# Performance work log

Measured on AMD Instinct MI355X. Metric: run time of the kernel, lower is better.

The kernel has to match this reference:

```python
import jax, jax.numpy as jnp
import numpy as np

DIM = 1024
HEADS = 16
HEAD_DIM = DIM // HEADS
MAX_SEQ = 4096
BATCH = 16
POSITION = MAX_SEQ - 1


def setup_inputs() -> dict:
    key = jax.random.key(0)
    ks = jax.random.split(key, 8)
    s = 0.02  # weight init scale, typical for transformer linears
    return {
        "token": jax.random.normal(ks[0], (BATCH, 1, DIM), dtype=jnp.float32),
        "k_cache": jax.random.normal(ks[1], (BATCH, MAX_SEQ, HEADS, HEAD_DIM), dtype=jnp.float32),
        "v_cache": jax.random.normal(ks[2], (BATCH, MAX_SEQ, HEADS, HEAD_DIM), dtype=jnp.float32),
        "Wq": jax.random.normal(ks[3], (DIM, DIM), dtype=jnp.float32) * s,
        "Wk": jax.random.normal(ks[4], (DIM, DIM), dtype=jnp.float32) * s,
        "Wv": jax.random.normal(ks[5], (DIM, DIM), dtype=jnp.float32) * s,
        "Wo": jax.random.normal(ks[6], (DIM, DIM), dtype=jnp.float32) * s,
        "position": POSITION,
    }


def reference(token, k_cache, v_cache, Wq, Wk, Wv, Wo, position):
    # Decode step: single-query attention against KV cache (FlexDecodingModule.decode).
    B = token.shape[0]
    # QKV projections (torch Linear: x @ W.T), bias=False
    q = (token @ Wq.T).reshape(B, 1, HEADS, HEAD_DIM)
    k = (token @ Wk.T).reshape(B, 1, HEADS, HEAD_DIM)
    v = (token @ Wv.T).reshape(B, 1, HEADS, HEAD_DIM)
    # Inline KV-cache append at `position` (static python int)
    kc = k_cache.at[:, position].set(k[:, 0])
    vc = v_cache.at[:, position].set(v[:, 0])
    past_k = kc[:, : position + 1]  # [B, L, H, D]
    past_v = vc[:, : position + 1]
    # Causal score_mod with offset=position, q_idx=0 => all kv_idx<=position visible (no mask)
    scale = 1.0 / np.sqrt(HEAD_DIM).astype(np.float32)
    scores = jnp.einsum("bqhd,bkhd->bhqk", q, past_k) * scale  # [B, H, 1, L]
    attn = jax.nn.softmax(scores, axis=-1)
    out = jnp.einsum("bhqk,bkhd->bqhd", attn, past_v)  # [B, 1, H, D]
    out = out.reshape(B, 1, DIM)
    return out @ Wo.T
```

## Files before the change

kernel.cpp:

```cpp
#include <hip/hip_runtime.h>
#include <hip/hip_bf16.h>
#include <math.h>

#define DIM 1024
#define HEADS 16
#define HEAD_DIM 64
#define MAXSEQ 4096
#define BATCH 16
#define CHUNK 64
#define NCHUNK (MAXSEQ / CHUNK)

__global__ __launch_bounds__(256) void qkv_proj(
    const float* __restrict__ token,
    const float* __restrict__ Wq, const float* __restrict__ Wk,
    const float* __restrict__ Wv,
    float* __restrict__ out ) {
  __shared__ float tok[BATCH * DIM];
  for (int idx = threadIdx.x; idx < BATCH * DIM; idx += 256)
    tok[idx] = token[idx];
  __syncthreads();

  const float* W = (blockIdx.y == 0) ? Wq : ((blockIdx.y == 1) ? Wk : Wv);
  float* o = out + (size_t)blockIdx.y * BATCH * DIM;

  const int wave = threadIdx.x >> 6;
  const int lane = threadIdx.x & 63;
  const int i0 = blockIdx.x * 16 + wave * 4;

  float acc[4][16];
#pragma unroll
  for (int ii = 0; ii < 4; ++ii)
#pragma unroll
    for (int b = 0; b < 16; ++b) acc[ii][b] = 0.f;

  for (int t = 0; t < 16; ++t) {
    const int j = t * 64 + lane;
    float tk[16];
#pragma unroll
    for (int b = 0; b < 16; ++b) tk[b] = tok[b * DIM + j];
#pragma unroll
    for (int ii = 0; ii < 4; ++ii) {
      const float w = W[(size_t)(i0 + ii) * DIM + j];
#pragma unroll
      for (int b = 0; b < 16; ++b) acc[ii][b] = fmaf(w, tk[b], acc[ii][b]);
    }
  }

#pragma unroll
  for (int ii = 0; ii < 4; ++ii)
#pragma unroll
    for (int b = 0; b < 16; ++b) {
      float v = acc[ii][b];
#pragma unroll
      for (int m = 32; m >= 1; m >>= 1) v += __shfl_xor(v, m);
      if (lane == 0) o[(size_t)b * DIM + i0 + ii] = v;
    }
}

__global__ __launch_bounds__(256) void attn_partial(
    const float* __restrict__ kc, const float* __restrict__ vc,
    const float* __restrict__ qkv, const int* __restrict__ pos_p,
    float* __restrict__ part) {
  const int c = blockIdx.x, b = blockIdx.y;
  const int t = threadIdx.x;
  const int h = t >> 4, lq = t & 15;
  const int pos = pos_p[0];
  const int nk = pos + 1;
  const int s0 = c * CHUNK;

  const float* qp   = qkv + (size_t)b * DIM;
  const float* knew = qkv + (size_t)BATCH * DIM + (size_t)b * DIM;
  const float* vnew = qkv + 2 * (size_t)BATCH * DIM + (size_t)b * DIM;
  const float* kbase = kc + (size_t)b * MAXSEQ * DIM;
  const float* vbase = vc + (size_t)b * MAXSEQ * DIM;

  const float scale = 0.125f;
  float4 q4 = *(const float4*)(qp + 4 * t);
  q4.x *= scale; q4.y *= scale; q4.z *= scale; q4.w *= scale;

  __shared__ float sc[CHUNK][17];

#pragma unroll 4
  for (int i = 0; i < CHUNK; ++i) {
    const int s = s0 + i;
    const bool valid = (s < nk);
    float d = 0.f;
    if (valid) {
      const float* krow = (s == pos) ? knew : (kbase + (size_t)s * DIM);
      const float4 k4 = *(const float4*)(krow + 4 * t);
      d = q4.x * k4.x + q4.y * k4.y + q4.z * k4.z + q4.w * k4.w;
      d += __shfl_xor(d, 1);
      d += __shfl_xor(d, 2);
      d += __shfl_xor(d, 4);
      d += __shfl_xor(d, 8);
    }
    if (lq == 0) sc[i][h] = valid ? d : -INFINITY;
  }
  __syncthreads();

  float m = -INFINITY;
#pragma unroll
  for (int r = 0; r < CHUNK / 16; ++r)
    m = fmaxf(m, sc[lq * (CHUNK / 16) + r][h]);
  m = fmaxf(m, __shfl_xor(m, 1));
  m = fmaxf(m, __shfl_xor(m, 2));
  m = fmaxf(m, __shfl_xor(m, 4));
  m = fmaxf(m, __shfl_xor(m, 8));

  float l = 0.f;
#pragma unroll
  for (int r = 0; r < CHUNK / 16; ++r) {
    const int i = lq * (CHUNK / 16) + r;
    const float sv = sc[i][h];
    const float p = (sv == -INFINITY) ? 0.f : __expf(sv - m);
    l += p;
    sc[i][h] = p;
  }
  l += __shfl_xor(l, 1);
  l += __shfl_xor(l, 2);
  l += __shfl_xor(l, 4);
  l += __shfl_xor(l, 8);
  __syncthreads();

  float4 a4 = make_float4(0.f, 0.f, 0.f, 0.f);
#pragma unroll 4
  for (int i = 0; i < CHUNK; ++i) {
    const int s = s0 + i;
    if (s < nk) {
      const float* vrow = (s == pos) ? vnew : (vbase + (size_t)s * DIM);
      const float4 v4 = *(const float4*)(vrow + 4 * t);
      const float p = sc[i][h];
      a4.x = fmaf(p, v4.x, a4.x);
      a4.y = fmaf(p, v4.y, a4.y);
      a4.z = fmaf(p, v4.z, a4.z);
      a4.w = fmaf(p, v4.w, a4.w);
    }
  }

  const size_t base = (((size_t)(b * HEADS + h)) * NCHUNK + c) * 66;
  part[base + 2 + lq * 4 + 0] = a4.x;
  part[base + 2 + lq * 4 + 1] = a4.y;
  part[base + 2 + lq * 4 + 2] = a4.z;
  part[base + 2 + lq * 4 + 3] = a4.w;
  if (lq == 0) { part[base] = m; part[base + 1] = l; }
}

__global__ __launch_bounds__(64) void attn_combine(
    const float* __restrict__ part, float* __restrict__ attn) {
  const int bh = blockIdx.x;
  const int b = bh >> 4, h = bh & 15;
  const int d = threadIdx.x;
  const float* p0 = part + (size_t)bh * NCHUNK * 66;
  float M = -INFINITY;
#pragma unroll
  for (int c = 0; c < NCHUNK; ++c) M = fmaxf(M, p0[c * 66]);
  float L = 0.f, o = 0.f;
#pragma unroll 8
  for (int c = 0; c < NCHUNK; ++c) {
    const float mc = p0[c * 66];
    if (mc > -INFINITY) {
      const float w = __expf(mc - M);
      L += p0[c * 66 + 1] * w;
      o = fmaf(p0[c * 66 + 2 + d], w, o);
    }
  }
  attn[(size_t)b * DIM + h * HEAD_DIM + d] = o / L;
}

__global__ __launch_bounds__(256) void o_proj(
    const float* __restrict__ attn, const float* __restrict__ Wo,
    float* __restrict__ out) {
  __shared__ float tok[BATCH * DIM];
  for (int idx = threadIdx.x; idx < BATCH * DIM; idx += 256)
    tok[idx] = attn[idx];
  __syncthreads();

  const int wave = threadIdx.x >> 6;
  const int lane = threadIdx.x & 63;
  const int i0 = blockIdx.x * 16 + wave * 4;

  float acc[4][16];
#pragma unroll
  for (int ii = 0; ii < 4; ++ii)
#pragma unroll
    for (int b = 0; b < 16; ++b) acc[ii][b] = 0.f;

  for (int t = 0; t < 16; ++t) {
    const int j = t * 64 + lane;
    float tk[16];
#pragma unroll
    for (int b = 0; b < 16; ++b) tk[b] = tok[b * DIM + j];
#pragma unroll
    for (int ii = 0; ii < 4; ++ii) {
      const float w = Wo[(size_t)(i0 + ii) * DIM + j];
#pragma unroll
      for (int b = 0; b < 16; ++b) acc[ii][b] = fmaf(w, tk[b], acc[ii][b]);
    }
  }

#pragma unroll
  for (int ii = 0; ii < 4; ++ii)
#pragma unroll
    for (int b = 0; b < 16; ++b) {
      float v = acc[ii][b];
#pragma unroll
      for (int m = 32; m >= 1; m >>= 1) v += __shfl_xor(v, m);
      if (lane == 0) out[(size_t)b * DIM + i0 + ii] = v;
    }
}

extern "C" void kernel_launch(void* const* d_in, const int* in_sizes, int n_in,
                              void* d_out, int out_size, void* d_ws, size_t ws_size,
                              hipStream_t stream) {
  const float* token = (const float*)d_in[0];
  const float* kc = (const float*)d_in[1];
  const float* vc = (const float*)d_in[2];
  const float* Wq = (const float*)d_in[3];
  const float* Wk = (const float*)d_in[4];
  const float* Wv = (const float*)d_in[5];
  const float* Wo = (const float*)d_in[6];
  const int* pos = (const int*)d_in[7];
  float* out = (float*)d_out;
  float* ws = (float*)d_ws;

  float* qkv = ws;
  float* part = ws + 3 * BATCH * DIM;
  float* attn = part + (size_t)BATCH * HEADS * NCHUNK * 66;

  hipLaunchKernelGGL(qkv_proj, dim3(64, 3), dim3(256), 0, stream,
                     token, Wq, Wk, Wv, qkv);
  hipLaunchKernelGGL(attn_partial, dim3(NCHUNK, BATCH), dim3(256), 0,
                     stream, kc, vc, qkv, pos, part);
  hipLaunchKernelGGL(attn_combine, dim3(BATCH * HEADS), dim3(64), 0, stream,
                     part, attn);
  hipLaunchKernelGGL(o_proj, dim3(64), dim3(256), 0, stream, attn, Wo, out);
  (void)in_sizes; (void)n_in; (void)out_size; (void)ws_size;
}
```

Baseline: 176.2 us.

## Fuse score, softmax and PV into single-pass online softmax with batched K/V loads

```diff
diff --git a/kernel.cpp b/kernel.cpp
--- a/kernel.cpp
+++ b/kernel.cpp
@@ -9,6 +9,7 @@
 #define BATCH 16
 #define CHUNK 64
 #define NCHUNK (MAXSEQ / CHUNK)
+#define TILE 8
 
 __global__ __launch_bounds__(256) void qkv_proj(
     const float* __restrict__ token,
@@ -78,62 +79,54 @@
   float4 q4 = *(const float4*)(qp + 4 * t);
   q4.x *= scale; q4.y *= scale; q4.z *= scale; q4.w *= scale;
 
-  __shared__ float sc[CHUNK][17];
-
-#pragma unroll 4
-  for (int i = 0; i < CHUNK; ++i) {
-    const int s = s0 + i;
-    const bool valid = (s < nk);
-    float d = 0.f;
-    if (valid) {
+  float m = -INFINITY, l = 0.f;
+  float4 a4 = make_float4(0.f, 0.f, 0.f, 0.f);
+
+  for (int i0 = 0; i0 < CHUNK; i0 += TILE) {
+    float4 k4[TILE], v4[TILE];
+#pragma unroll
+    for (int j = 0; j < TILE; ++j) {
+      const int s = s0 + i0 + j;
       const float* krow = (s == pos) ? knew : (kbase + (size_t)s * DIM);
-      const float4 k4 = *(const float4*)(krow + 4 * t);
-      d = q4.x * k4.x + q4.y * k4.y + q4.z * k4.z + q4.w * k4.w;
-      d += __shfl_xor(d, 1);
-      d += __shfl_xor(d, 2);
-      d += __shfl_xor(d, 4);
-      d += __shfl_xor(d, 8);
-    }
-    if (lq == 0) sc[i][h] = valid ? d : -INFINITY;
-  }
-  __syncthreads();
-
-  float m = -INFINITY;
-#pragma unroll
-  for (int r = 0; r < CHUNK / 16; ++r)
-    m = fmaxf(m, sc[lq * (CHUNK / 16) + r][h]);
-  m = fmaxf(m, __shfl_xor(m, 1));
-  m = fmaxf(m, __shfl_xor(m, 2));
-  m = fmaxf(m, __shfl_xor(m, 4));
-  m = fmaxf(m, __shfl_xor(m, 8));
-
-  float l = 0.f;
-#pragma unroll
-  for (int r = 0; r < CHUNK / 16; ++r) {
-    const int i = lq * (CHUNK / 16) + r;
-    const float sv = sc[i][h];
-    const float p = (sv == -INFINITY) ? 0.f : __expf(sv - m);
-    l += p;
-    sc[i][h] = p;
-  }
-  l += __shfl_xor(l, 1);
-  l += __shfl_xor(l, 2);
-  l += __shfl_xor(l, 4);
-  l += __shfl_xor(l, 8);
-  __syncthreads();
-
-  float4 a4 = make_float4(0.f, 0.f, 0.f, 0.f);
-#pragma unroll 4
-  for (int i = 0; i < CHUNK; ++i) {
-    const int s = s0 + i;
-    if (s < nk) {
       const float* vrow = (s == pos) ? vnew : (vbase + (size_t)s * DIM);
-      const float4 v4 = *(const float4*)(vrow + 4 * t);
-      const float p = sc[i][h];
-      a4.x = fmaf(p, v4.x, a4.x);
-      a4.y = fmaf(p, v4.y, a4.y);
-      a4.z = fmaf(p, v4.z, a4.z);
-      a4.w = fmaf(p, v4.w, a4.w);
+      k4[j] = *(const float4*)(krow + 4 * t);
+      v4[j] = *(const float4*)(vrow + 4 * t);
+    }
+
+    float sc[TILE];
+#pragma unroll
+    for (int j = 0; j < TILE; ++j)
+      sc[j] = q4.x * k4[j].x + q4.y * k4[j].y + q4.z * k4[j].z +
+              q4.w * k4[j].w;
+
+#pragma unroll
+    for (int j = 0; j < TILE; ++j) {
+      sc[j] += __shfl_xor(sc[j], 1);
+      sc[j] += __shfl_xor(sc[j], 2);
+      sc[j] += __shfl_xor(sc[j], 4);
+      sc[j] += __shfl_xor(sc[j], 8);
+    }
+#pragma unroll
+    for (int j = 0; j < TILE; ++j)
+      if (s0 + i0 + j >= nk) sc[j] = -INFINITY;
+
+    float tm = sc[0];
+#pragma unroll
+    for (int j = 1; j < TILE; ++j) tm = fmaxf(tm, sc[j]);
+    const float m_new = fmaxf(m, tm);
+    const float corr = (m_new == -INFINITY) ? 1.f : __expf(m - m_new);
+    l *= corr;
+    a4.x *= corr; a4.y *= corr; a4.z *= corr; a4.w *= corr;
+    m = m_new;
+
+#pragma unroll
+    for (int j = 0; j < TILE; ++j) {
+      const float p = (sc[j] == -INFINITY) ? 0.f : __expf(sc[j] - m);
+      l += p;
+      a4.x = fmaf(p, v4[j].x, a4.x);
+      a4.y = fmaf(p, v4[j].y, a4.y);
+      a4.z = fmaf(p, v4[j].z, a4.z);
+      a4.w = fmaf(p, v4[j].w, a4.w);
     }
   }
 
```

Result: faster. 167.2 us (-5.1%).
